# Optimization experiments

Hardware: AMD Instinct MI355X
Metric: run time of the kernel (lower is better)

The kernel has to match this reference:

```python
import jax, jax.numpy as jnp
import numpy as np

EPS = 1e-5
QMAX = 127.0


def fake_quant_int8(x):
    """Per-tensor symmetric int8 fake-quant (quantize+dequantize), dynamic scale.
    Mirrors brevitas Int8ActPerTensorFloat / Int8WeightPerTensorFloat math."""
    scale = jnp.maximum(jnp.max(jnp.abs(x)) / QMAX, 1e-8)
    q = jnp.clip(jnp.round(x / scale), -128.0, 127.0) * scale
    # straight-through estimator (identity grad through quant)
    return x + jax.lax.stop_gradient(q - x)


def layer_norm(x, g, b):
    mu = jnp.mean(x, axis=-1, keepdims=True)
    var = jnp.mean(jnp.square(x - mu), axis=-1, keepdims=True)
    return (x - mu) * jax.lax.rsqrt(var + EPS) * g + b


def setup_inputs() -> dict:
    key = jax.random.key(0)
    B, S, D, H = 64, 196, 768, 12
    M = 4 * D
    ks = jax.random.split(key, 8)
    s = lambda d: 1.0 / np.sqrt(d)
    return {
        "x": jax.random.normal(ks[0], (B, S, D), jnp.float32),
        "ln1_g": jnp.ones((D,), jnp.float32),
        "ln1_b": jnp.zeros((D,), jnp.float32),
        "ln2_g": jnp.ones((D,), jnp.float32),
        "ln2_b": jnp.zeros((D,), jnp.float32),
        "w_qkv": jax.random.normal(ks[1], (D, 3 * D), jnp.float32) * s(D),
        "b_qkv": jnp.zeros((3 * D,), jnp.float32),
        "w_o": jax.random.normal(ks[2], (D, D), jnp.float32) * s(D),
        "b_o": jnp.zeros((D,), jnp.float32),
        "w1": jax.random.normal(ks[3], (D, M), jnp.float32) * s(D),
        "b1": jnp.zeros((M,), jnp.float32),
        "w2": jax.random.normal(ks[4], (M, D), jnp.float32) * s(M),
        "b2": jnp.zeros((D,), jnp.float32),
    }


def _block(x, ln1_g, ln1_b, ln2_g, ln2_b, w_qkv, b_qkv, w_o, b_o, w1, b1, w2, b2):
    B, S, D = x.shape
    H = 12
    hd = D // H

    # --- LN -> quant -> MHSA -> add ---
    r1 = x
    h = fake_quant_int8(layer_norm(x, ln1_g, ln1_b))
    qkv = jnp.einsum("bsd,de->bse", h, fake_quant_int8(w_qkv)) + b_qkv
    q, k, v = jnp.split(qkv, 3, axis=-1)
    q = q.reshape(B, S, H, hd)
    k = k.reshape(B, S, H, hd)
    v = v.reshape(B, S, H, hd)
    logits = jnp.einsum("bqhd,bkhd->bhqk", q, k) / jnp.sqrt(jnp.float32(hd))
    attn = jax.nn.softmax(logits, axis=-1)
    ctx = jnp.einsum("bhqk,bkhd->bqhd", attn, v).reshape(B, S, D)
    ctx = fake_quant_int8(ctx)
    mhsa = jnp.einsum("bsd,de->bse", ctx, fake_quant_int8(w_o)) + b_o
    x = mhsa + r1

    # --- LN -> quant -> MLP (fc1 -> GELU -> quant -> fc2) -> add ---
    r2 = x
    h = fake_quant_int8(layer_norm(x, ln2_g, ln2_b))
    h = jnp.einsum("bsd,dm->bsm", h, fake_quant_int8(w1)) + b1
    h = jax.nn.gelu(h, approximate=False)  # torch nn.GELU default = exact erf
    h = fake_quant_int8(h)
    h = jnp.einsum("bsm,md->bsd", h, fake_quant_int8(w2)) + b2
    return h + r2


def reference(x, ln1_g, ln1_b, ln2_g, ln2_b, w_qkv, b_qkv, w_o, b_o, w1, b1, w2, b2):
    return _block(x, ln1_g, ln1_b, ln2_g, ln2_b, w_qkv, b_qkv, w_o, b_o, w1, b1, w2, b2)
```

## Files before the change

### kernel.cpp

```cpp
#include <hip/hip_runtime.h>
#include <cstdint>
#include <cstddef>

#define DEVFN __device__ __forceinline__

typedef short bf16x8 __attribute__((ext_vector_type(8)));
typedef float f32x4  __attribute__((ext_vector_type(4)));
typedef int   i32x4  __attribute__((ext_vector_type(4)));

static constexpr int NTOK  = 64 * 196;
static constexpr int DMODEL= 768;
static constexpr int NHEAD = 12;
static constexpr int NQKV  = 2304;
static constexpr int MMLP  = 3072;
static constexpr int SEQ   = 196;
static constexpr int NBATCH= 64;

enum { SL_LN1=0, SL_WQKV=1, SL_CTX=2, SL_WO=3, SL_LN2=4, SL_W1=5, SL_GELU=6, SL_W2=7 };

static constexpr int NSH       = 64;
static constexpr int SH_STRIDE = 64;
static constexpr int SLOTS_U32 = NSH * SH_STRIDE;

DEVFN float bf2f(unsigned short u){ return __uint_as_float(((unsigned)u) << 16); }
DEVFN unsigned cvt_pk_bf16(float a, float b){
  unsigned r;
  asm("v_cvt_pk_bf16_f32 %0, %1, %2" : "=v"(r) : "v"(a), "v"(b));
  return r;
}
DEVFN void split_pk(float a, float b, unsigned& hp, unsigned& lp){
  hp = cvt_pk_bf16(a, b);
  float ra = a - __uint_as_float(hp << 16);
  float rb = b - __uint_as_float(hp & 0xffff0000u);
  lp = cvt_pk_bf16(ra, rb);
}
DEVFN float slot_absmax(const unsigned* __restrict__ slots, int slot){
  unsigned m = 0u;
#pragma unroll
  for (int j = 0; j < NSH; j++){
    unsigned u = slots[j * SH_STRIDE + slot];
    m = (u > m) ? u : m;
  }
  return __uint_as_float(m);
}
DEVFN float slot_scale(const unsigned* __restrict__ slots, int slot){
  return fmaxf(slot_absmax(slots, slot) / 127.0f, 1e-8f);
}
DEVFN void scatter_amax(unsigned* slots, int slot, unsigned bucket, float v){
  atomicMax(slots + (bucket & (NSH - 1)) * SH_STRIDE + slot, __float_as_uint(v));
}
DEVFN float quantval(float x, float s){
  float q = rintf(x / s);
  return fminf(fmaxf(q, -128.0f), 127.0f);
}
DEVFN unsigned pack4(float a, float b, float c, float d){
  return  ((unsigned)(unsigned char)(char)(int)a)
        | ((unsigned)(unsigned char)(char)(int)b << 8)
        | ((unsigned)(unsigned char)(char)(int)c << 16)
        | ((unsigned)(unsigned char)(char)(int)d << 24);
}
DEVFN float gelu_fast(float v){
  float s  = v * 0.70710678118654752f;
  float ax = fabsf(s);
  float t  = __builtin_amdgcn_rcpf(fmaf(0.3275911f, ax, 1.0f));
  float p  = t * fmaf(t, fmaf(t, fmaf(t, fmaf(t, 1.061405429f, -1.453152027f),
                                      1.421413741f), -0.284496736f), 0.254829592f);
  float er = fmaf(-p, __expf(-ax * ax), 1.0f);
  unsigned sgn = __float_as_uint(s) & 0x80000000u;
  er = __uint_as_float(__float_as_uint(er) | sgn);
  return 0.5f * v * (1.0f + er);
}
DEVFN f32x4 mfma16(bf16x8 a, bf16x8 b, f32x4 c){
  return __builtin_amdgcn_mfma_f32_16x16x32_bf16(a, b, c, 0, 0, 0);
}
DEVFN i32x4 mfma16i8(i32x4 a, i32x4 b, i32x4 c){
  return __builtin_amdgcn_mfma_i32_16x16x64_i8(a, b, c, 0, 0, 0);
}
DEVFN void async_ld16(const void* g, void* lds){
  __builtin_amdgcn_global_load_lds((const __attribute__((address_space(1))) void*)g,
                                   (__attribute__((address_space(3))) void*)lds, 16, 0, 0);
}
DEVFN int vidx(int d, int s){
  return d * 256 + (s ^ (((d ^ (d >> 2)) & 7) << 3));
}
DEVFN void xcd_swizzle(int gx, int gy, int& bx, int& by){
  int nwg = gx * gy;
  int bid = blockIdx.y * gx + blockIdx.x;
  int q = nwg >> 3, r = nwg & 7;
  int xcd = bid & 7, loc = bid >> 3;
  int sw = (xcd < r) ? (xcd * (q + 1) + loc) : (r * (q + 1) + (xcd - r) * q + loc);
  bx = sw % gx; by = sw / gx;
}

__global__ void k_init(unsigned* slots){
  int i = blockIdx.x * blockDim.x + threadIdx.x;
  if (i < SLOTS_U32) slots[i] = 0u;
}

__global__ void k_absmax4(const float* __restrict__ x0, const float* __restrict__ x1,
                          const float* __restrict__ x2, const float* __restrict__ x3,
                          unsigned* slots){
  int bid = blockIdx.x;
  const float* x; int n4, slot, b0, nb;
  if (bid < 256)      { x = x0; n4 = DMODEL * NQKV  / 4; slot = SL_WQKV; b0 = 0;   nb = 256; }
  else if (bid < 384) { x = x1; n4 = DMODEL * DMODEL/ 4; slot = SL_WO;   b0 = 256; nb = 128; }
  else if (bid < 640) { x = x2; n4 = DMODEL * MMLP  / 4; slot = SL_W1;   b0 = 384; nb = 256; }
  else                { x = x3; n4 = MMLP   * DMODEL/ 4; slot = SL_W2;   b0 = 640; nb = 256; }
  int lb = bid - b0;
  float m = 0.f;
  const float4* x4 = (const float4*)x;
  int stride = nb * blockDim.x;
  for (int j = lb * blockDim.x + threadIdx.x; j < n4; j += stride){
    float4 v = x4[j];
    m = fmaxf(m, fmaxf(fmaxf(fabsf(v.x), fabsf(v.y)), fmaxf(fabsf(v.z), fabsf(v.w))));
  }
  for (int off = 32; off; off >>= 1) m = fmaxf(m, __shfl_xor(m, off));
  __shared__ float wm[4];
  int lane = threadIdx.x & 63, w = threadIdx.x >> 6;
  if (lane == 0) wm[w] = m;
  __syncthreads();
  if (threadIdx.x == 0){
    float bm = fmaxf(fmaxf(wm[0], wm[1]), fmaxf(wm[2], wm[3]));
    scatter_amax(slots, slot, bid, bm);
  }
}

__global__ void k_quant_transpose4(const float* __restrict__ w0, const float* __restrict__ w1,
                                   const float* __restrict__ w2, const float* __restrict__ w3,
                                   char* __restrict__ t0, char* __restrict__ t1,
                                   char* __restrict__ t2, char* __restrict__ t3,
                                   const unsigned* __restrict__ slots){
  int bid = blockIdx.x;
  const float* w; char* wt; int K, N, slot, lb;
  if (bid < 1728)      { w = w0; wt = t0; K = DMODEL; N = NQKV;   slot = SL_WQKV; lb = bid; }
  else if (bid < 2304) { w = w1; wt = t1; K = DMODEL; N = DMODEL; slot = SL_WO;   lb = bid - 1728; }
  else if (bid < 4608) { w = w2; wt = t2; K = DMODEL; N = MMLP;   slot = SL_W1;   lb = bid - 2304; }
  else                 { w = w3; wt = t3; K = MMLP;   N = DMODEL; slot = SL_W2;   lb = bid - 4608; }
  int nx = N / 32;
  int bx = lb % nx, by = lb / nx;

  __shared__ float tile[32][33];
  float s = slot_scale(slots, slot);
  int n0 = bx * 32, k0 = by * 32;
  int tx = threadIdx.x & 31, ty = threadIdx.x >> 5;
#pragma unroll
  for (int i = 0; i < 4; i++){
    int k = k0 + ty + i * 8;
    float v = w[(size_t)k * N + n0 + tx];
    tile[ty + i * 8][tx] = quantval(v, s);
  }
  __syncthreads();
  int n = threadIdx.x >> 3, kg = threadIdx.x & 7;
  unsigned o = pack4(tile[kg * 4 + 0][n], tile[kg * 4 + 1][n],
                     tile[kg * 4 + 2][n], tile[kg * 4 + 3][n]);
  *(unsigned*)(wt + (size_t)(n0 + n) * K + k0 + kg * 4) = o;
}

__global__ void k_layernorm(const float* __restrict__ x, const float* __restrict__ g,
                            const float* __restrict__ b, float* __restrict__ out,
                            unsigned* slots, int slot){
  int w = threadIdx.x >> 6, lane = threadIdx.x & 63;
  int row = blockIdx.x * 4 + w;
  const float4* xr = (const float4*)(x + (size_t)row * DMODEL);
  float4 v[3];
  float sum = 0.f;
#pragma unroll
  for (int i = 0; i < 3; i++){ v[i] = xr[i * 64 + lane]; sum += v[i].x + v[i].y + v[i].z + v[i].w; }
  for (int off = 32; off; off >>= 1) sum += __shfl_xor(sum, off);
  float mu = sum * (1.0f / 768.0f);
  float vs = 0.f;
#pragma unroll
  for (int i = 0; i < 3; i++){
    float dx = v[i].x - mu, dy = v[i].y - mu, dz = v[i].z - mu, dw = v[i].w - mu;
    vs += dx * dx + dy * dy + dz * dz + dw * dw;
  }
  for (int off = 32; off; off >>= 1) vs += __shfl_xor(vs, off);
  float inv = 1.0f / sqrtf(vs * (1.0f / 768.0f) + 1e-5f);
  const float4* g4 = (const float4*)g; const float4* b4 = (const float4*)b;
  float4* o4 = (float4*)(out + (size_t)row * DMODEL);
  float am = 0.f;
#pragma unroll
  for (int i = 0; i < 3; i++){
    float4 gg = g4[i * 64 + lane], bb = b4[i * 64 + lane], o;
    o.x = (v[i].x - mu) * inv * gg.x + bb.x;
    o.y = (v[i].y - mu) * inv * gg.y + bb.y;
    o.z = (v[i].z - mu) * inv * gg.z + bb.z;
    o.w = (v[i].w - mu) * inv * gg.w + bb.w;
    am = fmaxf(am, fmaxf(fmaxf(fabsf(o.x), fabsf(o.y)), fmaxf(fabsf(o.z), fabsf(o.w))));
    o4[i * 64 + lane] = o;
  }
  for (int off = 32; off; off >>= 1) am = fmaxf(am, __shfl_xor(am, off));
  __shared__ float am4[4];
  if (lane == 0) am4[w] = am;
  __syncthreads();
  if (threadIdx.x == 0){
    float bm = fmaxf(fmaxf(am4[0], am4[1]), fmaxf(am4[2], am4[3]));
    scatter_amax(slots, slot, blockIdx.x, bm);
  }
}

__global__ void k_quant_act(const float* __restrict__ x, unsigned* __restrict__ out,
                            int n4, const unsigned* __restrict__ slots, int slot){
  float s = slot_scale(slots, slot);
  const float4* x4 = (const float4*)x;
  int stride = gridDim.x * blockDim.x;
  for (int j = blockIdx.x * blockDim.x + threadIdx.x; j < n4; j += stride){
    float4 v = x4[j];
    out[j] = pack4(quantval(v.x, s), quantval(v.y, s), quantval(v.z, s), quantval(v.w, s));
  }
}

__global__ void k_quant_bf16_i8(const unsigned short* __restrict__ x, unsigned* __restrict__ out,
                                int n4, const unsigned* __restrict__ slots, int slot){
  float s = slot_scale(slots, slot);
  const ushort4* x4 = (const ushort4*)x;
  int stride = gridDim.x * blockDim.x;
  for (int j = blockIdx.x * blockDim.x + threadIdx.x; j < n4; j += stride){
    ushort4 v = x4[j];
    out[j] = pack4(quantval(bf2f(v.x), s), quantval(bf2f(v.y), s),
                   quantval(bf2f(v.z), s), quantval(bf2f(v.w), s));
  }
}

template<int EPI>
__launch_bounds__(256, 4)
__global__ void k_gemm(const char* __restrict__ A,
                       const char* __restrict__ Bt,
                       const float* __restrict__ bias,
                       const float* __restrict__ res,
                       float* __restrict__ Cf,
                       unsigned short* __restrict__ Cb,
                       const unsigned* __restrict__ slots, int sa_slot, int sb_slot,
                       unsigned* gmax_slots, int gmax_slot,
                       int M, int N, int K)
{
  __shared__ __align__(16) char smem[32768];
  __shared__ float gm4[4];
  const int tid  = threadIdx.x;
  const int lane = tid & 63;
  const int wv   = tid >> 6;
  const int wx   = wv & 1, wy = wv >> 1;
  const int quad = lane >> 4;
  const int l16  = lane & 15;
  int bx, by;
  xcd_swizzle(gridDim.x, gridDim.y, bx, by);
  const int m0 = by * 128, n0 = bx * 128;

  auto issue = [&](int k0, int buf){
#pragma unroll
    for (int i = 0; i < 2; i++){
      int c = tid + i * 256;
      int row = c >> 2, q = c & 3;
      int qs = (q - ((row + (row >> 2)) & 3)) & 3;
      async_ld16(A + (size_t)(m0 + row) * K + k0 + qs * 16,
                 smem + buf * 8192 + (i * 256 + wv * 64) * 16);
    }
#pragma unroll
    for (int i = 0; i < 2; i++){
      int c = tid + i * 256;
      int row = c >> 2, q = c & 3;
      int qs = (q - ((row + (row >> 2)) & 3)) & 3;
      async_ld16(Bt + (size_t)(n0 + row) * K + k0 + qs * 16,
                 smem + 16384 + buf * 8192 + (i * 256 + wv * 64) * 16);
    }
  };

  i32x4 acc[4][4] = {};
  const int nk = K >> 6;
  issue(0, 0);

  const int ch = (((quad + (l16 & 3) + (l16 >> 2)) & 3)) * 16;

  for (int k = 0; k < nk; k++){
    const int cur = k & 1;
    if (k + 1 < nk){
      issue((k + 1) << 6, cur ^ 1);
      asm volatile("s_waitcnt vmcnt(4)" ::: "memory");
    } else {
      asm volatile("s_waitcnt vmcnt(0)" ::: "memory");
    }
    asm volatile("s_barrier" ::: "memory");

    const char* Ab = smem + cur * 8192;
    const char* Bb = smem + 16384 + cur * 8192;
    i32x4 af[4], bfr[4];
#pragma unroll
    for (int i = 0; i < 4; i++)
      af[i] = *(const i32x4*)(Ab + (wy * 64 + i * 16 + l16) * 64 + ch);
#pragma unroll
    for (int j = 0; j < 4; j++)
      bfr[j] = *(const i32x4*)(Bb + (wx * 64 + j * 16 + l16) * 64 + ch);
    asm volatile("s_waitcnt lgkmcnt(0)" ::: "memory");
    asm volatile("s_barrier" ::: "memory");

#pragma unroll
    for (int i = 0; i < 4; i++)
#pragma unroll
      for (int j = 0; j < 4; j++)
        acc[i][j] = mfma16i8(af[i], bfr[j], acc[i][j]);
  }
  __syncthreads();

  float (*stage)[132] = (float (*)[132])smem;
  const float sc = slot_scale(slots, sa_slot) * slot_scale(slots, sb_slot);
  const int col4 = (tid & 31) * 4;
  const int gc   = n0 + col4;
  const float4 bb = *(const float4*)&bias[gc];
  float gmax = 0.f;
#pragma unroll
  for (int i = 0; i < 4; i++){
#pragma unroll
    for (int j = 0; j < 4; j++)
#pragma unroll
      for (int r = 0; r < 4; r++)
        stage[wy * 16 + quad * 4 + r][wx * 64 + j * 16 + l16] = (float)acc[i][j][r];
    __syncthreads();
#pragma unroll
    for (int rr = 0; rr < 4; rr++){
      const int rl = rr * 8 + (tid >> 5);
      const int gm = m0 + ((rl >> 4) * 64) + i * 16 + (rl & 15);
      float4 v = *(const float4*)&stage[rl][col4];
      v.x = v.x * sc + bb.x; v.y = v.y * sc + bb.y;
      v.z = v.z * sc + bb.z; v.w = v.w * sc + bb.w;
      if constexpr (EPI == 1){
        float4 rv = *(const float4*)&res[(size_t)gm * N + gc];
        v.x += rv.x; v.y += rv.y; v.z += rv.z; v.w += rv.w;
        *(float4*)&Cf[(size_t)gm * N + gc] = v;
      } else if constexpr (EPI == 2){
        float g0 = gelu_fast(v.x);
        float g1 = gelu_fast(v.y);
        float g2 = gelu_fast(v.z);
        float g3 = gelu_fast(v.w);
        gmax = fmaxf(gmax, fmaxf(fmaxf(fabsf(g0), fabsf(g1)), fmaxf(fabsf(g2), fabsf(g3))));
        uint2 o = {cvt_pk_bf16(g0, g1), cvt_pk_bf16(g2, g3)};
        *(uint2*)&Cb[(size_t)gm * N + gc] = o;
      } else {
        *(float4*)&Cf[(size_t)gm * N + gc] = v;
      }
    }
    __syncthreads();
  }
  if constexpr (EPI == 2){
    for (int off = 32; off; off >>= 1) gmax = fmaxf(gmax, __shfl_xor(gmax, off));
    if (lane == 0) gm4[wv] = gmax;
    __syncthreads();
    if (tid == 0){
      float bm = fmaxf(fmaxf(gm4[0], gm4[1]), fmaxf(gm4[2], gm4[3]));
      scatter_amax(gmax_slots, gmax_slot, blockIdx.x + blockIdx.y * gridDim.x, bm);
    }
  }
}

__launch_bounds__(832, 4)
__global__ void k_attention(const float* __restrict__ qkv, float* __restrict__ ctx,
                            unsigned* slots){
  __shared__ __align__(16) unsigned short Khi[208 * 72], Klo[208 * 72];
  __shared__ __align__(16) unsigned short Vhi[64 * 256], Vlo[64 * 256];
  __shared__ __align__(16) unsigned short Ps[13][2][16 * 40];
  __shared__ float gm[13];

  const int bh = blockIdx.x;
  const int b = bh / NHEAD, h = bh % NHEAD;
  const float* base = qkv + (size_t)b * SEQ * NQKV;
  const int tid = threadIdx.x, lane = tid & 63, wv = tid >> 6;
  const int quad = lane >> 4, l16 = lane & 15;

  float4 kreg[4], vreg[5];
#pragma unroll
  for (int i = 0; i < 4; i++){
    int idx = tid + i * 832;
    int r = idx >> 4, c4 = (idx & 15) * 4;
    float4 v = {0.f, 0.f, 0.f, 0.f};
    if (r < SEQ) v = *(const float4*)(base + (size_t)r * NQKV + DMODEL + h * 64 + c4);
    kreg[i] = v;
  }
#pragma unroll
  for (int i = 0; i < 5; i++){
    int idx = tid + i * 832;
    int s = idx >> 4, dg = (idx & 15) * 4;
    float4 v = {0.f, 0.f, 0.f, 0.f};
    if (idx < 232 * 16 && s < SEQ)
      v = *(const float4*)(base + (size_t)s * NQKV + 2 * DMODEL + h * 64 + dg);
    vreg[i] = v;
  }
#pragma unroll
  for (int i = 0; i < 4; i++){
    int idx = tid + i * 832;
    int r = idx >> 4, c4 = (idx & 15) * 4;
    float4 v = kreg[i];
    unsigned h01, l01, h23, l23;
    split_pk(v.x, v.y, h01, l01);
    split_pk(v.z, v.w, h23, l23);
    *(uint2*)(Khi + r * 72 + c4) = uint2{h01, h23};
    *(uint2*)(Klo + r * 72 + c4) = uint2{l01, l23};
  }
#pragma unroll
  for (int i = 0; i < 5; i++){
    int idx = tid + i * 832;
    if (idx < 232 * 16){
      int s = idx >> 4, dg = (idx & 15) * 4;
      float4 v = vreg[i];
      unsigned h01, l01, h23, l23;
      split_pk(v.x, v.y, h01, l01);
      split_pk(v.z, v.w, h23, l23);
      Vhi[vidx(dg + 0, s)] = (unsigned short)h01; Vhi[vidx(dg + 1, s)] = (unsigned short)(h01 >> 16);
      Vhi[vidx(dg + 2, s)] = (unsigned short)h23; Vhi[vidx(dg + 3, s)] = (unsigned short)(h23 >> 16);
      Vlo[vidx(dg + 0, s)] = (unsigned short)l01; Vlo[vidx(dg + 1, s)] = (unsigned short)(l01 >> 16);
      Vlo[vidx(dg + 2, s)] = (unsigned short)l23; Vlo[vidx(dg + 3, s)] = (unsigned short)(l23 >> 16);
    }
  }
  __syncthreads();

  unsigned short* PsH = &Ps[wv][0][0];
  unsigned short* PsL = &Ps[wv][1][0];

  float gmax = 0.f;
  const int qt = wv;
  {
    const int q0 = qt * 16;
    const int sq = q0 + l16;
    const bool valid = sq < SEQ;

    bf16x8 aqh[2], aql[2];
    const float* qrow = base + (size_t)(valid ? sq : 0) * NQKV + h * 64;
#pragma unroll
    for (int ks = 0; ks < 2; ks++){
      float4 v0 = {0,0,0,0}, v1 = {0,0,0,0};
      if (valid){
        v0 = *(const float4*)(qrow + ks * 32 + quad * 8);
        v1 = *(const float4*)(qrow + ks * 32 + quad * 8 + 4);
      }
      unsigned* ah = (unsigned*)&aqh[ks];
      unsigned* al = (unsigned*)&aql[ks];
      split_pk(v0.x, v0.y, ah[0], al[0]);
      split_pk(v0.z, v0.w, ah[1], al[1]);
      split_pk(v1.x, v1.y, ah[2], al[2]);
      split_pk(v1.z, v1.w, ah[3], al[3]);
    }

    f32x4 sacc[13];
    __builtin_amdgcn_s_setprio(1);
#pragma unroll
    for (int t = 0; t < 13; t++){
      f32x4 a = {0.f, 0.f, 0.f, 0.f};
#pragma unroll
      for (int ks = 0; ks < 2; ks++){
        bf16x8 bkh = *(const bf16x8*)(Khi + (t * 16 + l16) * 72 + ks * 32 + quad * 8);
        bf16x8 bkl = *(const bf16x8*)(Klo + (t * 16 + l16) * 72 + ks * 32 + quad * 8);
        a = mfma16(aqh[ks], bkh, a);
        a = mfma16(aqh[ks], bkl, a);
        a = mfma16(aql[ks], bkh, a);
      }
      sacc[t] = a;
    }
    __builtin_amdgcn_s_setprio(0);

    float mx[4] = {-1e30f, -1e30f, -1e30f, -1e30f};
#pragma unroll
    for (int t = 0; t < 13; t++){
      bool dead = (t == 12) && (l16 >= 4);
#pragma unroll
      for (int r = 0; r < 4; r++){
        float v = dead ? -1e30f : sacc[t][r] * 0.125f;
        sacc[t][r] = v;
        mx[r] = fmaxf(mx[r], v);
      }
    }
#pragma unroll
    for (int off = 1; off < 16; off <<= 1)
#pragma unroll
      for (int r = 0; r < 4; r++) mx[r] = fmaxf(mx[r], __shfl_xor(mx[r], off));
    float sum[4] = {0.f, 0.f, 0.f, 0.f};
#pragma unroll
    for (int t = 0; t < 13; t++)
#pragma unroll
      for (int r = 0; r < 4; r++){
        float e = __expf(sacc[t][r] - mx[r]);
        sacc[t][r] = e; sum[r] += e;
      }
#pragma unroll
    for (int off = 1; off < 16; off <<= 1)
#pragma unroll
      for (int r = 0; r < 4; r++) sum[r] += __shfl_xor(sum[r], off);
    float inv[4];
#pragma unroll
    for (int r = 0; r < 4; r++) inv[r] = 1.0f / sum[r];

    f32x4 oacc[4] = {};
#pragma unroll
    for (int ks = 0; ks < 7; ks++){
      const int t0 = 2 * ks, t1 = 2 * ks + 1;
#pragma unroll
      for (int r = 0; r < 4; r++){
        int row = quad * 4 + r;
        float a = sacc[t0][r] * inv[r];
        float c = (t1 < 13) ? sacc[t1][r] * inv[r] : 0.f;
        unsigned hp, lp;
        split_pk(a, c, hp, lp);
        PsH[row * 40 + l16]      = (unsigned short)hp;
        PsH[row * 40 + 16 + l16] = (unsigned short)(hp >> 16);
        PsL[row * 40 + l16]      = (unsigned short)lp;
        PsL[row * 40 + 16 + l16] = (unsigned short)(lp >> 16);
      }
      __builtin_amdgcn_wave_barrier();
      bf16x8 aph = *(const bf16x8*)(PsH + l16 * 40 + quad * 8);
      bf16x8 apl = *(const bf16x8*)(PsL + l16 * 40 + quad * 8);
      __builtin_amdgcn_s_setprio(1);
#pragma unroll
      for (int n = 0; n < 4; n++){
        bf16x8 bvh = *(const bf16x8*)(Vhi + vidx(n * 16 + l16, ks * 32 + quad * 8));
        bf16x8 bvl = *(const bf16x8*)(Vlo + vidx(n * 16 + l16, ks * 32 + quad * 8));
        oacc[n] = mfma16(aph, bvh, oacc[n]);
        oacc[n] = mfma16(aph, bvl, oacc[n]);
        oacc[n] = mfma16(apl, bvh, oacc[n]);
      }
      __builtin_amdgcn_s_setprio(0);
      __builtin_amdgcn_wave_barrier();
    }

#pragma unroll
    for (int r = 0; r < 4; r++){
      int srow = q0 + quad * 4 + r;
      if (srow < SEQ){
#pragma unroll
        for (int n = 0; n < 4; n++){
          float v = oacc[n][r];
          ctx[((size_t)(b * SEQ + srow)) * DMODEL + h * 64 + n * 16 + l16] = v;
          gmax = fmaxf(gmax, fabsf(v));
        }
      }
    }
  }
  for (int off = 32; off; off >>= 1) gmax = fmaxf(gmax, __shfl_xor(gmax, off));
  if (lane == 0) gm[wv] = gmax;
  __syncthreads();
  if (tid == 0){
    float bm = 0.f;
#pragma unroll
    for (int i = 0; i < 13; i++) bm = fmaxf(bm, gm[i]);
    scatter_amax(slots, SL_CTX, blockIdx.x, bm);
  }
}

extern "C" void kernel_launch(void* const* d_in, const int* in_sizes, int n_in,
                              void* d_out, int out_size, void* d_ws, size_t ws_size,
                              hipStream_t stream)
{
  const float* x     = (const float*)d_in[0];
  const float* ln1_g = (const float*)d_in[1];
  const float* ln1_b = (const float*)d_in[2];
  const float* ln2_g = (const float*)d_in[3];
  const float* ln2_b = (const float*)d_in[4];
  const float* w_qkv = (const float*)d_in[5];
  const float* b_qkv = (const float*)d_in[6];
  const float* w_o   = (const float*)d_in[7];
  const float* b_o   = (const float*)d_in[8];
  const float* w1    = (const float*)d_in[9];
  const float* b1    = (const float*)d_in[10];
  const float* w2    = (const float*)d_in[11];
  const float* b2    = (const float*)d_in[12];

  char* ws = (char*)d_ws;
  size_t off = 0;
  unsigned* slots = (unsigned*)ws;                 off += SLOTS_U32 * 4;
  char* wqkvT = (char*)(ws + off); off += (size_t)NQKV  * DMODEL;
  char* woT   = (char*)(ws + off); off += (size_t)DMODEL* DMODEL;
  char* w1T   = (char*)(ws + off); off += (size_t)MMLP  * DMODEL;
  char* w2T   = (char*)(ws + off); off += (size_t)DMODEL* MMLP;
  off = (off + 255) & ~(size_t)255;
  float* t1    = (float*)(ws + off);               off += (size_t)NTOK * DMODEL * 4;
  char*  t1q   = (char*)(ws + off);                off += (size_t)NTOK * DMODEL;
  off = (off + 255) & ~(size_t)255;
  float* qkv   = (float*)(ws + off);               off += (size_t)NTOK * NQKV * 4;
  float* xmid  = (float*)(ws + off);               off += (size_t)NTOK * DMODEL * 4;
  unsigned short* h1 = (unsigned short*)qkv;
  char* h1q = (char*)qkv + (size_t)NTOK * MMLP * 2;
  float* outp = (float*)d_out;

  k_init<<<(SLOTS_U32 + 255) / 256, 256, 0, stream>>>(slots);

  k_absmax4<<<896, 256, 0, stream>>>(w_qkv, w_o, w1, w2, slots);

  k_quant_transpose4<<<6912, 256, 0, stream>>>(w_qkv, w_o, w1, w2,
                                               wqkvT, woT, w1T, w2T, slots);

  k_layernorm<<<NTOK / 4, 256, 0, stream>>>(x, ln1_g, ln1_b, t1, slots, SL_LN1);
  {
    int n4 = NTOK * DMODEL / 4;
    k_quant_act<<<2048, 256, 0, stream>>>(t1, (unsigned*)t1q, n4, slots, SL_LN1);
  }
  k_gemm<0><<<dim3(NQKV / 128, NTOK / 128), 256, 0, stream>>>(
      t1q, wqkvT, b_qkv, nullptr, qkv, nullptr, slots, SL_LN1, SL_WQKV, nullptr, 0,
      NTOK, NQKV, DMODEL);

  k_attention<<<NBATCH * NHEAD, 832, 0, stream>>>(qkv, t1, slots);
  {
    int n4 = NTOK * DMODEL / 4;
    k_quant_act<<<2048, 256, 0, stream>>>(t1, (unsigned*)t1q, n4, slots, SL_CTX);
  }
  k_gemm<1><<<dim3(DMODEL / 128, NTOK / 128), 256, 0, stream>>>(
      t1q, woT, b_o, x, xmid, nullptr, slots, SL_CTX, SL_WO, nullptr, 0,
      NTOK, DMODEL, DMODEL);

  k_layernorm<<<NTOK / 4, 256, 0, stream>>>(xmid, ln2_g, ln2_b, t1, slots, SL_LN2);
  {
    int n4 = NTOK * DMODEL / 4;
    k_quant_act<<<2048, 256, 0, stream>>>(t1, (unsigned*)t1q, n4, slots, SL_LN2);
  }
  k_gemm<2><<<dim3(MMLP / 128, NTOK / 128), 256, 0, stream>>>(
      t1q, w1T, b1, nullptr, nullptr, h1, slots, SL_LN2, SL_W1, slots, SL_GELU,
      NTOK, MMLP, DMODEL);
  {
    int n4 = NTOK * MMLP / 4;
    k_quant_bf16_i8<<<2048, 256, 0, stream>>>(h1, (unsigned*)h1q, n4, slots, SL_GELU);
  }
  k_gemm<1><<<dim3(DMODEL / 128, NTOK / 128), 256, 0, stream>>>(
      h1q, w2T, b2, xmid, outp, nullptr, slots, SL_GELU, SL_W2, nullptr, 0,
      NTOK, DMODEL, MMLP);
}
```

Baseline: 443.5 us.

## Recompute LayerNorm from stats instead of storing fp32, merge prep kernels

LayerNorm is split into a stats pass (mean, inv-std and absmax) and a recompute-and-quantize pass that writes int8 directly. This removes the fp32 normalized-activation write and its re-read by a separate quant kernel. The LN1 stats and quant passes are merged into the weight absmax and weight quant-transpose kernels to cut launches, and the slot-init kernel becomes a memset. Attention block indices are remapped across XCDs. The cost is reading x twice instead of writing and reading a full fp32 intermediate.

```diff
diff --git a/kernel.cpp b/kernel.cpp
--- a/kernel.cpp
+++ b/kernel.cpp
@@ -92,75 +92,9 @@
   bx = sw % gx; by = sw / gx;
 }
 
-__global__ void k_init(unsigned* slots){
-  int i = blockIdx.x * blockDim.x + threadIdx.x;
-  if (i < SLOTS_U32) slots[i] = 0u;
-}
-
-__global__ void k_absmax4(const float* __restrict__ x0, const float* __restrict__ x1,
-                          const float* __restrict__ x2, const float* __restrict__ x3,
-                          unsigned* slots){
-  int bid = blockIdx.x;
-  const float* x; int n4, slot, b0, nb;
-  if (bid < 256)      { x = x0; n4 = DMODEL * NQKV  / 4; slot = SL_WQKV; b0 = 0;   nb = 256; }
-  else if (bid < 384) { x = x1; n4 = DMODEL * DMODEL/ 4; slot = SL_WO;   b0 = 256; nb = 128; }
-  else if (bid < 640) { x = x2; n4 = DMODEL * MMLP  / 4; slot = SL_W1;   b0 = 384; nb = 256; }
-  else                { x = x3; n4 = MMLP   * DMODEL/ 4; slot = SL_W2;   b0 = 640; nb = 256; }
-  int lb = bid - b0;
-  float m = 0.f;
-  const float4* x4 = (const float4*)x;
-  int stride = nb * blockDim.x;
-  for (int j = lb * blockDim.x + threadIdx.x; j < n4; j += stride){
-    float4 v = x4[j];
-    m = fmaxf(m, fmaxf(fmaxf(fabsf(v.x), fabsf(v.y)), fmaxf(fabsf(v.z), fabsf(v.w))));
-  }
-  for (int off = 32; off; off >>= 1) m = fmaxf(m, __shfl_xor(m, off));
-  __shared__ float wm[4];
-  int lane = threadIdx.x & 63, w = threadIdx.x >> 6;
-  if (lane == 0) wm[w] = m;
-  __syncthreads();
-  if (threadIdx.x == 0){
-    float bm = fmaxf(fmaxf(wm[0], wm[1]), fmaxf(wm[2], wm[3]));
-    scatter_amax(slots, slot, bid, bm);
-  }
-}
-
-__global__ void k_quant_transpose4(const float* __restrict__ w0, const float* __restrict__ w1,
-                                   const float* __restrict__ w2, const float* __restrict__ w3,
-                                   char* __restrict__ t0, char* __restrict__ t1,
-                                   char* __restrict__ t2, char* __restrict__ t3,
-                                   const unsigned* __restrict__ slots){
-  int bid = blockIdx.x;
-  const float* w; char* wt; int K, N, slot, lb;
-  if (bid < 1728)      { w = w0; wt = t0; K = DMODEL; N = NQKV;   slot = SL_WQKV; lb = bid; }
-  else if (bid < 2304) { w = w1; wt = t1; K = DMODEL; N = DMODEL; slot = SL_WO;   lb = bid - 1728; }
-  else if (bid < 4608) { w = w2; wt = t2; K = DMODEL; N = MMLP;   slot = SL_W1;   lb = bid - 2304; }
-  else                 { w = w3; wt = t3; K = MMLP;   N = DMODEL; slot = SL_W2;   lb = bid - 4608; }
-  int nx = N / 32;
-  int bx = lb % nx, by = lb / nx;
-
-  __shared__ float tile[32][33];
-  float s = slot_scale(slots, slot);
-  int n0 = bx * 32, k0 = by * 32;
-  int tx = threadIdx.x & 31, ty = threadIdx.x >> 5;
-#pragma unroll
-  for (int i = 0; i < 4; i++){
-    int k = k0 + ty + i * 8;
-    float v = w[(size_t)k * N + n0 + tx];
-    tile[ty + i * 8][tx] = quantval(v, s);
-  }
-  __syncthreads();
-  int n = threadIdx.x >> 3, kg = threadIdx.x & 7;
-  unsigned o = pack4(tile[kg * 4 + 0][n], tile[kg * 4 + 1][n],
-                     tile[kg * 4 + 2][n], tile[kg * 4 + 3][n]);
-  *(unsigned*)(wt + (size_t)(n0 + n) * K + k0 + kg * 4) = o;
-}
-
-__global__ void k_layernorm(const float* __restrict__ x, const float* __restrict__ g,
-                            const float* __restrict__ b, float* __restrict__ out,
-                            unsigned* slots, int slot){
-  int w = threadIdx.x >> 6, lane = threadIdx.x & 63;
-  int row = blockIdx.x * 4 + w;
+DEVFN float ln_stats_wave(const float* __restrict__ x, const float* __restrict__ g,
+                          const float* __restrict__ b, float2* __restrict__ stats,
+                          int row, int lane){
   const float4* xr = (const float4*)(x + (size_t)row * DMODEL);
   float4 v[3];
   float sum = 0.f;
@@ -177,18 +111,46 @@
   for (int off = 32; off; off >>= 1) vs += __shfl_xor(vs, off);
   float inv = 1.0f / sqrtf(vs * (1.0f / 768.0f) + 1e-5f);
   const float4* g4 = (const float4*)g; const float4* b4 = (const float4*)b;
-  float4* o4 = (float4*)(out + (size_t)row * DMODEL);
   float am = 0.f;
 #pragma unroll
   for (int i = 0; i < 3; i++){
-    float4 gg = g4[i * 64 + lane], bb = b4[i * 64 + lane], o;
-    o.x = (v[i].x - mu) * inv * gg.x + bb.x;
-    o.y = (v[i].y - mu) * inv * gg.y + bb.y;
-    o.z = (v[i].z - mu) * inv * gg.z + bb.z;
-    o.w = (v[i].w - mu) * inv * gg.w + bb.w;
-    am = fmaxf(am, fmaxf(fmaxf(fabsf(o.x), fabsf(o.y)), fmaxf(fabsf(o.z), fabsf(o.w))));
-    o4[i * 64 + lane] = o;
-  }
+    float4 gg = g4[i * 64 + lane], bb = b4[i * 64 + lane];
+    float ox = (v[i].x - mu) * inv * gg.x + bb.x;
+    float oy = (v[i].y - mu) * inv * gg.y + bb.y;
+    float oz = (v[i].z - mu) * inv * gg.z + bb.z;
+    float ow = (v[i].w - mu) * inv * gg.w + bb.w;
+    am = fmaxf(am, fmaxf(fmaxf(fabsf(ox), fabsf(oy)), fmaxf(fabsf(oz), fabsf(ow))));
+  }
+  if (lane == 0) stats[row] = float2{mu, inv};
+  return am;
+}
+DEVFN void ln_quant_wave(const float* __restrict__ x, const float* __restrict__ g,
+                         const float* __restrict__ b, const float2* __restrict__ stats,
+                         char* __restrict__ outq, float s, int row, int lane){
+  float2 st = stats[row];
+  float mu = st.x, inv = st.y;
+  const float4* xr = (const float4*)(x + (size_t)row * DMODEL);
+  const float4* g4 = (const float4*)g; const float4* b4 = (const float4*)b;
+  unsigned* oq = (unsigned*)(outq + (size_t)row * DMODEL);
+#pragma unroll
+  for (int i = 0; i < 3; i++){
+    float4 v = xr[i * 64 + lane];
+    float4 gg = g4[i * 64 + lane], bb = b4[i * 64 + lane];
+    float ox = (v.x - mu) * inv * gg.x + bb.x;
+    float oy = (v.y - mu) * inv * gg.y + bb.y;
+    float oz = (v.z - mu) * inv * gg.z + bb.z;
+    float ow = (v.w - mu) * inv * gg.w + bb.w;
+    oq[i * 64 + lane] = pack4(quantval(ox, s), quantval(oy, s),
+                              quantval(oz, s), quantval(ow, s));
+  }
+}
+
+__global__ void k_ln_stats(const float* __restrict__ x, const float* __restrict__ g,
+                           const float* __restrict__ b, float2* __restrict__ stats,
+                           unsigned* slots, int slot){
+  int w = threadIdx.x >> 6, lane = threadIdx.x & 63;
+  int row = blockIdx.x * 4 + w;
+  float am = ln_stats_wave(x, g, b, stats, row, lane);
   for (int off = 32; off; off >>= 1) am = fmaxf(am, __shfl_xor(am, off));
   __shared__ float am4[4];
   if (lane == 0) am4[w] = am;
@@ -196,6 +158,95 @@
   if (threadIdx.x == 0){
     float bm = fmaxf(fmaxf(am4[0], am4[1]), fmaxf(am4[2], am4[3]));
     scatter_amax(slots, slot, blockIdx.x, bm);
+  }
+}
+__global__ void k_ln_quant(const float* __restrict__ x, const float* __restrict__ g,
+                           const float* __restrict__ b, const float2* __restrict__ stats,
+                           char* __restrict__ outq, const unsigned* __restrict__ slots, int slot){
+  int w = threadIdx.x >> 6, lane = threadIdx.x & 63;
+  int row = blockIdx.x * 4 + w;
+  float s = slot_scale(slots, slot);
+  ln_quant_wave(x, g, b, stats, outq, s, row, lane);
+}
+
+__global__ void k_prep1(const float* __restrict__ w_qkv, const float* __restrict__ w_o,
+                        const float* __restrict__ w1, const float* __restrict__ w2,
+                        const float* __restrict__ x, const float* __restrict__ g,
+                        const float* __restrict__ b, float2* __restrict__ stats,
+                        unsigned* slots){
+  __shared__ float red[4];
+  int bid = blockIdx.x;
+  int lane = threadIdx.x & 63, w = threadIdx.x >> 6;
+  if (bid < 896){
+    const float* xx; int n4, slot, b0, nb;
+    if (bid < 256)      { xx = w_qkv; n4 = DMODEL * NQKV  / 4; slot = SL_WQKV; b0 = 0;   nb = 256; }
+    else if (bid < 384) { xx = w_o;   n4 = DMODEL * DMODEL/ 4; slot = SL_WO;   b0 = 256; nb = 128; }
+    else if (bid < 640) { xx = w1;    n4 = DMODEL * MMLP  / 4; slot = SL_W1;   b0 = 384; nb = 256; }
+    else                { xx = w2;    n4 = MMLP   * DMODEL/ 4; slot = SL_W2;   b0 = 640; nb = 256; }
+    int lb = bid - b0;
+    float m = 0.f;
+    const float4* x4 = (const float4*)xx;
+    int stride = nb * blockDim.x;
+    for (int j = lb * blockDim.x + threadIdx.x; j < n4; j += stride){
+      float4 v = x4[j];
+      m = fmaxf(m, fmaxf(fmaxf(fabsf(v.x), fabsf(v.y)), fmaxf(fabsf(v.z), fabsf(v.w))));
+    }
+    for (int off = 32; off; off >>= 1) m = fmaxf(m, __shfl_xor(m, off));
+    if (lane == 0) red[w] = m;
+    __syncthreads();
+    if (threadIdx.x == 0){
+      float bm = fmaxf(fmaxf(red[0], red[1]), fmaxf(red[2], red[3]));
+      scatter_amax(slots, slot, bid, bm);
+    }
+  } else {
+    int row = (bid - 896) * 4 + w;
+    float am = ln_stats_wave(x, g, b, stats, row, lane);
+    for (int off = 32; off; off >>= 1) am = fmaxf(am, __shfl_xor(am, off));
+    if (lane == 0) red[w] = am;
+    __syncthreads();
+    if (threadIdx.x == 0){
+      float bm = fmaxf(fmaxf(red[0], red[1]), fmaxf(red[2], red[3]));
+      scatter_amax(slots, SL_LN1, bid, bm);
+    }
+  }
+}
+
+__global__ void k_prep2(const float* __restrict__ w0, const float* __restrict__ w1,
+                        const float* __restrict__ w2, const float* __restrict__ w3,
+                        char* __restrict__ t0, char* __restrict__ t1,
+                        char* __restrict__ t2, char* __restrict__ t3,
+                        const float* __restrict__ x, const float* __restrict__ g,
+                        const float* __restrict__ b, const float2* __restrict__ stats,
+                        char* __restrict__ outq, const unsigned* __restrict__ slots){
+  __shared__ float tile[32][33];
+  int bid = blockIdx.x;
+  if (bid < 6912){
+    const float* w; char* wt; int K, N, slot, lb;
+    if (bid < 1728)      { w = w0; wt = t0; K = DMODEL; N = NQKV;   slot = SL_WQKV; lb = bid; }
+    else if (bid < 2304) { w = w1; wt = t1; K = DMODEL; N = DMODEL; slot = SL_WO;   lb = bid - 1728; }
+    else if (bid < 4608) { w = w2; wt = t2; K = DMODEL; N = MMLP;   slot = SL_W1;   lb = bid - 2304; }
+    else                 { w = w3; wt = t3; K = MMLP;   N = DMODEL; slot = SL_W2;   lb = bid - 4608; }
+    int nx = N / 32;
+    int bx = lb % nx, by = lb / nx;
+    float s = slot_scale(slots, slot);
+    int n0 = bx * 32, k0 = by * 32;
+    int tx = threadIdx.x & 31, ty = threadIdx.x >> 5;
+#pragma unroll
+    for (int i = 0; i < 4; i++){
+      int k = k0 + ty + i * 8;
+      float v = w[(size_t)k * N + n0 + tx];
+      tile[ty + i * 8][tx] = quantval(v, s);
+    }
+    __syncthreads();
+    int n = threadIdx.x >> 3, kg = threadIdx.x & 7;
+    unsigned o = pack4(tile[kg * 4 + 0][n], tile[kg * 4 + 1][n],
+                       tile[kg * 4 + 2][n], tile[kg * 4 + 3][n]);
+    *(unsigned*)(wt + (size_t)(n0 + n) * K + k0 + kg * 4) = o;
+  } else {
+    int w = threadIdx.x >> 6, lane = threadIdx.x & 63;
+    int row = (bid - 6912) * 4 + w;
+    float s = slot_scale(slots, SL_LN1);
+    ln_quant_wave(x, g, b, stats, outq, s, row, lane);
   }
 }
 
@@ -359,7 +410,7 @@
   __shared__ __align__(16) unsigned short Ps[13][2][16 * 40];
   __shared__ float gm[13];
 
-  const int bh = blockIdx.x;
+  const int bh = ((blockIdx.x & 7) * 96) + (blockIdx.x >> 3);
   const int b = bh / NHEAD, h = bh % NHEAD;
   const float* base = qkv + (size_t)b * SEQ * NQKV;
   const int tid = threadIdx.x, lane = tid & 63, wv = tid >> 6;
@@ -563,6 +614,7 @@
   char* ws = (char*)d_ws;
   size_t off = 0;
   unsigned* slots = (unsigned*)ws;                 off += SLOTS_U32 * 4;
+  float2* stats = (float2*)(ws + off);             off += (size_t)NTOK * 8;
   char* wqkvT = (char*)(ws + off); off += (size_t)NQKV  * DMODEL;
   char* woT   = (char*)(ws + off); off += (size_t)DMODEL* DMODEL;
   char* w1T   = (char*)(ws + off); off += (size_t)MMLP  * DMODEL;
@@ -577,18 +629,12 @@
   char* h1q = (char*)qkv + (size_t)NTOK * MMLP * 2;
   float* outp = (float*)d_out;
 
-  k_init<<<(SLOTS_U32 + 255) / 256, 256, 0, stream>>>(slots);
-
-  k_absmax4<<<896, 256, 0, stream>>>(w_qkv, w_o, w1, w2, slots);
-
-  k_quant_transpose4<<<6912, 256, 0, stream>>>(w_qkv, w_o, w1, w2,
-                                               wqkvT, woT, w1T, w2T, slots);
-
-  k_layernorm<<<NTOK / 4, 256, 0, stream>>>(x, ln1_g, ln1_b, t1, slots, SL_LN1);
-  {
-    int n4 = NTOK * DMODEL / 4;
-    k_quant_act<<<2048, 256, 0, stream>>>(t1, (unsigned*)t1q, n4, slots, SL_LN1);
-  }
+  hipMemsetAsync(slots, 0, SLOTS_U32 * 4, stream);
+
+  k_prep1<<<4032, 256, 0, stream>>>(w_qkv, w_o, w1, w2, x, ln1_g, ln1_b, stats, slots);
+  k_prep2<<<10048, 256, 0, stream>>>(w_qkv, w_o, w1, w2, wqkvT, woT, w1T, w2T,
+                                     x, ln1_g, ln1_b, stats, t1q, slots);
+
   k_gemm<0><<<dim3(NQKV / 128, NTOK / 128), 256, 0, stream>>>(
       t1q, wqkvT, b_qkv, nullptr, qkv, nullptr, slots, SL_LN1, SL_WQKV, nullptr, 0,
       NTOK, NQKV, DMODEL);
@@ -602,11 +648,9 @@
       t1q, woT, b_o, x, xmid, nullptr, slots, SL_CTX, SL_WO, nullptr, 0,
       NTOK, DMODEL, DMODEL);
 
-  k_layernorm<<<NTOK / 4, 256, 0, stream>>>(xmid, ln2_g, ln2_b, t1, slots, SL_LN2);
-  {
-    int n4 = NTOK * DMODEL / 4;
-    k_quant_act<<<2048, 256, 0, stream>>>(t1, (unsigned*)t1q, n4, slots, SL_LN2);
-  }
+  k_ln_stats<<<NTOK / 4, 256, 0, stream>>>(xmid, ln2_g, ln2_b, stats, slots, SL_LN2);
+  k_ln_quant<<<NTOK / 4, 256, 0, stream>>>(xmid, ln2_g, ln2_b, stats, t1q, slots, SL_LN2);
+
   k_gemm<2><<<dim3(MMLP / 128, NTOK / 128), 256, 0, stream>>>(
       t1q, w1T, b1, nullptr, nullptr, h1, slots, SL_LN2, SL_W1, slots, SL_GELU,
       NTOK, MMLP, DMODEL);
```

After: 432.8 us (median of 2 runs). 2.4% less time.
